# Performance work log

Measured on AMD Instinct MI355X. Metric: run time of the kernel, lower is better.

## Reference

```python
import jax, jax.numpy as jnp
import numpy as np

N_HEAD = 12
HEAD_DIM = 64
ROPE_THETA = 10000.0


def _rope_tables(t):
    half = HEAD_DIM // 2
    inv_freq = 1.0 / (ROPE_THETA ** (jnp.arange(0, HEAD_DIM, 2, dtype=jnp.float32) / HEAD_DIM))
    freqs = jnp.arange(t, dtype=jnp.float32)[:, None] * inv_freq[None, :]  # [t, half]
    return jnp.cos(freqs), jnp.sin(freqs)


def _apply_rope(q, k, cos, sin):
    # q,k: [b,h,t,d]; cos,sin: [t,d/2]
    half = HEAD_DIM // 2
    c = cos[None, None]
    s = sin[None, None]
    q1, q2 = q[..., :half], q[..., half:]
    k1, k2 = k[..., :half], k[..., half:]
    q = jnp.concatenate([q1 * c - q2 * s, q2 * c + q1 * s], axis=-1)
    k = jnp.concatenate([k1 * c - k2 * s, k2 * c + k1 * s], axis=-1)
    return q, k


def setup_inputs() -> dict:
    key = jax.random.key(0)
    ks = jax.random.split(key, 5)
    b, t, c = 1, 2048, 768
    return {
        "x": jax.random.normal(ks[0], (b, t, c), dtype=jnp.float32),
        "w_qkv": jax.random.normal(ks[1], (c, 3 * c), dtype=jnp.float32) * (1.0 / np.sqrt(c)),
        "b_qkv": jax.random.normal(ks[2], (3 * c,), dtype=jnp.float32) * 0.02,
        "w_proj": jax.random.normal(ks[3], (c, c), dtype=jnp.float32) * (1.0 / np.sqrt(c)),
        "b_proj": jax.random.normal(ks[4], (c,), dtype=jnp.float32) * 0.02,
    }


def reference(x, w_qkv, b_qkv, w_proj, b_proj):
    b, t, c = x.shape
    scale = 1.0 / np.sqrt(HEAD_DIM)
    qkv = jnp.einsum('btc,cd->btd', x, w_qkv) + b_qkv  # [b,t,3c]
    q, k, v = jnp.split(qkv, 3, axis=-1)
    # [b,t,c] -> [b,h,t,d]
    to_heads = lambda z: z.reshape(b, t, N_HEAD, HEAD_DIM).transpose(0, 2, 1, 3)
    q, k, v = to_heads(q), to_heads(k), to_heads(v)
    cos, sin = _rope_tables(t)
    q, k = _apply_rope(q, k, cos, sin)
    att = jnp.einsum('bhqd,bhkd->bhqk', q, k) * scale
    causal = jnp.tril(jnp.ones((t, t), dtype=bool))
    att = jnp.where(causal[None, None], att, -jnp.inf)
    att = jax.nn.softmax(att, axis=-1)
    y = jnp.einsum('bhqk,bhkd->bhqd', att, v)
    y = y.transpose(0, 2, 1, 3).reshape(b, t, c)
    return jnp.einsum('btc,cd->btd', y, w_proj) + b_proj
```

## Files before the change

### kernel.cpp

```cpp
#include <hip/hip_runtime.h>
#include <hip/hip_bf16.h>
#include <math.h>

#define T_SEQ 2048
#define C_DIM 768
#define NH    12
#define HD    64
#define QKV_N 2304
#define CH    4
#define NJOBS 1728

typedef __attribute__((ext_vector_type(8))) short short8;
typedef __attribute__((ext_vector_type(4))) short short4_t;
typedef __attribute__((ext_vector_type(4))) float f32x4;
typedef __hip_bfloat16 bf16;

static __device__ __forceinline__ unsigned int f2bf(float x) {
    bf16 b = __float2bfloat16(x);
    return (unsigned int)*reinterpret_cast<unsigned short*>(&b);
}
static __device__ __forceinline__ float bf2f(short u) {
    unsigned int v = ((unsigned int)(unsigned short)u) << 16;
    return *reinterpret_cast<float*>(&v);
}

static __device__ __forceinline__ void gload_lds16(const void* g, void* l) {
    __builtin_amdgcn_global_load_lds(
        (const __attribute__((address_space(1))) void*)g,
        (__attribute__((address_space(3))) void*)l, 16, 0, 0);
}

static __device__ __forceinline__ void transpose_tile(
    const float* __restrict__ W, short* __restrict__ Wt, int K, int N,
    int bx, int by, float* tile ) {
    int k0 = by * 64, n0 = bx * 64;
    int tid = threadIdx.x;
    #pragma unroll
    for (int e = 0; e < 16; ++e) {
        int idx = e * 256 + tid;
        int r = idx >> 6, c = idx & 63;
        tile[r * 65 + c] = W[(size_t)(k0 + r) * N + n0 + c];
    }
    __syncthreads();
    #pragma unroll
    for (int e = 0; e < 16; ++e) {
        int idx = e * 256 + tid;
        int n = idx >> 6, k = idx & 63;
        Wt[(size_t)(n0 + n) * K + k0 + k] = (short)f2bf(tile[k * 65 + n]);
    }
}

__global__ __launch_bounds__(256) void prep_kernel(
    const float* __restrict__ x, const float* __restrict__ w_qkv,
    const float* __restrict__ w_proj, short* __restrict__ xb,
    short* __restrict__ wqkvT, short* __restrict__ wprojT,
    float* __restrict__ ctab, float* __restrict__ stab) {
    __shared__ float tile[64 * 65];
    int b = blockIdx.x;
    int tid = threadIdx.x;
    if (b < 1536) {
        int idx = (b * 256 + tid) * 4;
        float4 v = *(const float4*)(x + idx);
        short4_t o;
        o[0] = (short)f2bf(v.x); o[1] = (short)f2bf(v.y);
        o[2] = (short)f2bf(v.z); o[3] = (short)f2bf(v.w);
        *(short4_t*)(xb + idx) = o;
    } else if (b < 1968) {
        int i = b - 1536;
        transpose_tile(w_qkv, wqkvT, C_DIM, QKV_N, i % 36, i / 36, tile);
    } else if (b < 2112) {
        int i = b - 1968;
        transpose_tile(w_proj, wprojT, C_DIM, C_DIM, i % 12, i / 12, tile);
    } else {
        int idx = (b - 2112) * 256 + tid;
        int p = idx >> 5;
        int i = idx & 31;
        float invf = exp2f(-(float)i * (0.03125f * 13.287712379549449f));
        float f = (float)p * invf;
        ctab[idx] = cosf(f);
        stab[idx] = sinf(f);
    }
}

__global__ __launch_bounds__(256) void gemm_qkv_rope_kernel(
    const short* __restrict__ A, const short* __restrict__ Bt,
    const float* __restrict__ bias, const float* __restrict__ ctab,
    const float* __restrict__ stab, short* __restrict__ Qout,
    short* __restrict__ Kout, short* __restrict__ Vtout) {
    __shared__ __align__(16) short smem[2 * 8 * 130 * 8];
    short* As = smem;
    short* Bs = smem + 8 * 130 * 8;
    int tid = threadIdx.x;
    int w = tid >> 6, l = tid & 63;
    int lr = l & 15, lg = l >> 4;
    int wm = w >> 1, wn = w & 1;
    int m0 = blockIdx.y * 128, n0 = blockIdx.x * 128;
    const int K = C_DIM;

    f32x4 acc[4][4] = {};

    for (int k0 = 0; k0 < K; k0 += 64) {
        __syncthreads();
        #pragma unroll
        for (int e = 0; e < 4; ++e) {
            int u = w * 4 + e;
            int kc = u >> 1, r0 = (u & 1) * 64;
            const short* srcA = A  + (size_t)(m0 + r0 + l) * K + k0 + kc * 8;
            const short* srcB = Bt + (size_t)(n0 + r0 + l) * K + k0 + kc * 8;
            gload_lds16(srcA, &As[(kc * 130 + r0) * 8]);
            gload_lds16(srcB, &Bs[(kc * 130 + r0) * 8]);
        }
        __syncthreads();
        #pragma unroll
        for (int ks = 0; ks < 2; ++ks) {
            short8 af[4], bf[4];
            #pragma unroll
            for (int mt = 0; mt < 4; ++mt)
                af[mt] = *(const short8*)&As[((ks * 4 + lg) * 130 + wm * 64 + mt * 16 + lr) * 8];
            #pragma unroll
            for (int nt = 0; nt < 4; ++nt)
                bf[nt] = *(const short8*)&Bs[((ks * 4 + lg) * 130 + wn * 64 + nt * 16 + lr) * 8];
            #pragma unroll
            for (int mt = 0; mt < 4; ++mt)
                #pragma unroll
                for (int nt = 0; nt < 4; ++nt)
                    acc[mt][nt] = __builtin_amdgcn_mfma_f32_16x16x32_bf16(
                        af[mt], bf[nt], acc[mt][nt], 0, 0, 0);
        }
    }

    __syncthreads();

    int nc0 = n0 + wn * 64;
    int tensor = nc0 / 768;
    int h = (nc0 - tensor * 768) >> 6;
    int t0g = m0 + wm * 64;

    float bv[4];
    #pragma unroll
    for (int nt = 0; nt < 4; ++nt) bv[nt] = bias[nc0 + nt * 16 + lr];

    if (tensor < 2) {
        short* dst = (tensor == 0 ? Qout : Kout) + (size_t)h * T_SEQ * HD;
        float qs = (tensor == 0) ? 0.125f : 1.0f;
        #pragma unroll
        for (int mt = 0; mt < 4; ++mt)
            #pragma unroll
            for (int r = 0; r < 4; ++r) {
                int t = t0g + mt * 16 + lg * 4 + r;
                #pragma unroll
                for (int nt = 0; nt < 2; ++nt) {
                    int i = nt * 16 + lr;
                    float c = ctab[t * 32 + i];
                    float s = stab[t * 32 + i];
                    float lo = acc[mt][nt][r]     + bv[nt];
                    float hi = acc[mt][nt + 2][r] + bv[nt + 2];
                    dst[(size_t)t * HD + i]      = (short)f2bf((lo * c - hi * s) * qs);
                    dst[(size_t)t * HD + i + 32] = (short)f2bf((hi * c + lo * s) * qs);
                }
            }
    } else {
        short* S = smem + w * 4096;
        #pragma unroll
        for (int mt = 0; mt < 4; ++mt)
            #pragma unroll
            for (int nt = 0; nt < 4; ++nt) {
                int d = nt * 16 + lr;
                #pragma unroll
                for (int r = 0; r < 4; ++r) {
                    int tl = mt * 16 + lg * 4 + r;
                    float v = acc[mt][nt][r] + bv[nt];
                    S[d * 64 + ((tl & 7) | (((tl >> 3) ^ (d & 7)) << 3))] =
                        (short)f2bf(v);
                }
            }
        asm volatile("s_waitcnt lgkmcnt(0)" ::: "memory");
        int cc = l & 7, db = l >> 3;
        #pragma unroll
        for (int i = 0; i < 8; ++i) {
            int d = db + i * 8;
            short8 v = *(const short8*)&S[d * 64 + ((cc ^ (d & 7)) << 3)];
            *(short8*)(Vtout + ((size_t)h * HD + d) * T_SEQ + t0g + cc * 8) = v;
        }
    }
}

__global__ __launch_bounds__(256) void gemm_proj_kernel(
    const short* __restrict__ A, const short* __restrict__ Bt,
    const float* __restrict__ bias, float* __restrict__ C) {
    const int K = C_DIM, N = C_DIM;
    __shared__ __align__(16) short As[8 * 66 * 8];
    __shared__ __align__(16) short Bs[8 * 66 * 8];
    int tid = threadIdx.x;
    int w = tid >> 6, l = tid & 63;
    int lr = l & 15, lg = l >> 4;
    int wm = w >> 1, wn = w & 1;
    int m0 = blockIdx.y * 64, n0 = blockIdx.x * 64;

    f32x4 acc[2][2] = {};

    for (int k0 = 0; k0 < K; k0 += 64) {
        __syncthreads();
        #pragma unroll
        for (int e = 0; e < 2; ++e) {
            int kc = w * 2 + e;
            gload_lds16(A  + (size_t)(m0 + l) * K + k0 + kc * 8, &As[kc * 66 * 8]);
            gload_lds16(Bt + (size_t)(n0 + l) * K + k0 + kc * 8, &Bs[kc * 66 * 8]);
        }
        __syncthreads();
        #pragma unroll
        for (int ks = 0; ks < 2; ++ks) {
            short8 af[2], bf[2];
            #pragma unroll
            for (int mt = 0; mt < 2; ++mt)
                af[mt] = *(const short8*)&As[((ks * 4 + lg) * 66 + wm * 32 + mt * 16 + lr) * 8];
            #pragma unroll
            for (int nt = 0; nt < 2; ++nt)
                bf[nt] = *(const short8*)&Bs[((ks * 4 + lg) * 66 + wn * 32 + nt * 16 + lr) * 8];
            #pragma unroll
            for (int mt = 0; mt < 2; ++mt)
                #pragma unroll
                for (int nt = 0; nt < 2; ++nt)
                    acc[mt][nt] = __builtin_amdgcn_mfma_f32_16x16x32_bf16(
                        af[mt], bf[nt], acc[mt][nt], 0, 0, 0);
        }
    }

    #pragma unroll
    for (int mt = 0; mt < 2; ++mt)
        #pragma unroll
        for (int r = 0; r < 4; ++r) {
            int row = m0 + wm * 32 + mt * 16 + lg * 4 + r;
            #pragma unroll
            for (int nt = 0; nt < 2; ++nt) {
                int col = n0 + wn * 32 + nt * 16 + lr;
                C[(size_t)row * N + col] = acc[mt][nt][r] + bias[col];
            }
        }
}

__global__ __launch_bounds__(256) void attn_mfma_kernel(
    const bf16* __restrict__ Qp, const bf16* __restrict__ Kp,
    const bf16* __restrict__ Vtp, short* __restrict__ Yb,
    short* __restrict__ Opart, float* __restrict__ ml) {
    __shared__ __align__(16) short KsB[2][64 * 64];
    __shared__ __align__(16) short VtB[2][64 * 64];
    __shared__ __align__(16) short Pl[4][16 * 64];

    int tid = threadIdx.x;
    int w  = tid >> 6;
    int l  = tid & 63;
    int lr = l & 15;
    int lg = l >> 4;

    int job = (NJOBS - 1) - blockIdx.x;
    int h = job % NH;
    int u = job / NH;
    int g = 0;
    while (u >= 2 * (g + 1) * (g + 2)) ++g;
    int v  = u - 2 * g * (g + 1);
    int jq = v / (g + 1);
    int qi = 4 * g + jq;
    int c0 = v - jq * (g + 1);
    int nch = g + 1;
    int kt0 = c0 * CH;
    int kt1 = kt0 + CH; if (kt1 > qi + 1) kt1 = qi + 1;
    int qt0 = qi * 64;

    const short* Qg  = (const short*)(Qp + (size_t)h * T_SEQ * HD);
    const short* Kg  = (const short*)(Kp + (size_t)h * T_SEQ * HD);
    const short* Vtg = (const short*)(Vtp + (size_t)h * HD * T_SEQ);

    int qrow = qt0 + w * 16 + lr;
    short8 qf0 = *(const short8*)(Qg + (size_t)qrow * HD + lg * 8);
    short8 qf1 = *(const short8*)(Qg + (size_t)qrow * HD + 32 + lg * 8);

    int srow = l >> 3;
    int cx   = (l & 7) ^ srow;

    auto stage = [&](int buf, int kt) {
        int k0 = kt * 64;
        #pragma unroll
        for (int e = 0; e < 2; ++e) {
            int r = e * 32 + w * 8 + srow;
            gload_lds16(Kg + (size_t)(k0 + r) * HD + cx * 8,
                        &KsB[buf][(e * 256 + w * 64) * 8]);
            gload_lds16(Vtg + (size_t)r * T_SEQ + k0 + cx * 8,
                        &VtB[buf][(e * 256 + w * 64) * 8]);
        }
    };

    f32x4 o[4] = {};
    float m = -INFINITY, lsum = 0.f;

    stage(0, kt0);

    for (int kt = kt0; kt < kt1; ++kt) {
        int cur = (kt - kt0) & 1;
        if (kt + 1 < kt1) {
            stage(1 - cur, kt + 1);
            asm volatile("s_waitcnt vmcnt(4)" ::: "memory");
        } else {
            asm volatile("s_waitcnt vmcnt(0)" ::: "memory");
        }
        __builtin_amdgcn_s_barrier();

        const short* Ks = KsB[cur];
        const short* Vt = VtB[cur];

        f32x4 c[4];
        #pragma unroll
        for (int mt = 0; mt < 4; ++mt) {
            c[mt] = (f32x4){0.f, 0.f, 0.f, 0.f};
            int row = mt * 16 + lr;
            #pragma unroll
            for (int ks = 0; ks < 2; ++ks) {
                short8 af = *(const short8*)(&Ks[row * 64 + (((ks * 4 + lg) ^ (row & 7)) << 3)]);
                c[mt] = __builtin_amdgcn_mfma_f32_16x16x32_bf16(af, ks ? qf1 : qf0, c[mt], 0, 0, 0);
            }
        }

        float p[16];
        float smax = -INFINITY;
        if (kt == qi) {
            int qg = qt0 + w * 16 + lr;
            int k0 = kt * 64;
            #pragma unroll
            for (int mt = 0; mt < 4; ++mt)
                #pragma unroll
                for (int r = 0; r < 4; ++r) {
                    float s = c[mt][r];
                    if (k0 + mt * 16 + lg * 4 + r > qg) s = -INFINITY;
                    p[mt * 4 + r] = s;
                    smax = fmaxf(smax, s);
                }
        } else {
            #pragma unroll
            for (int mt = 0; mt < 4; ++mt)
                #pragma unroll
                for (int r = 0; r < 4; ++r) {
                    float s = c[mt][r];
                    p[mt * 4 + r] = s;
                    smax = fmaxf(smax, s);
                }
        }
        smax = fmaxf(smax, __shfl_xor(smax, 16));
        smax = fmaxf(smax, __shfl_xor(smax, 32));
        float mnew = fmaxf(m, smax);
        float alpha = __expf(m - mnew);
        float ps = 0.f;
        #pragma unroll
        for (int i = 0; i < 16; ++i) { p[i] = __expf(p[i] - mnew); ps += p[i]; }
        ps += __shfl_xor(ps, 16);
        ps += __shfl_xor(ps, 32);
        lsum = lsum * alpha + ps;
        m = mnew;

        #pragma unroll
        for (int r = 0; r < 4; ++r) {
            float ar = __shfl(alpha, lg * 4 + r);
            #pragma unroll
            for (int nt = 0; nt < 4; ++nt) o[nt][r] *= ar;
        }

        short* Pw = &Pl[w][0];
        #pragma unroll
        for (int mt = 0; mt < 4; ++mt)
            #pragma unroll
            for (int rh = 0; rh < 2; ++rh) {
                unsigned int uu = f2bf(p[mt * 4 + 2 * rh]) | (f2bf(p[mt * 4 + 2 * rh + 1]) << 16);
                int chunk = 2 * mt + (lg >> 1);
                *(unsigned int*)(&Pw[lr * 64 + ((chunk ^ (lr & 7)) << 3)
                                     + 4 * (lg & 1) + 2 * rh]) = uu;
            }
        asm volatile("" ::: "memory");

        #pragma unroll
        for (int ks = 0; ks < 2; ++ks) {
            short8 pf = *(const short8*)(&Pw[lr * 64 + (((ks * 4 + lg) ^ (lr & 7)) << 3)]);
            #pragma unroll
            for (int nt = 0; nt < 4; ++nt) {
                int vrow = nt * 16 + lr;
                short8 vf = *(const short8*)(&Vt[vrow * 64 + (((ks * 4 + lg) ^ (vrow & 7)) << 3)]);
                o[nt] = __builtin_amdgcn_mfma_f32_16x16x32_bf16(pf, vf, o[nt], 0, 0, 0);
            }
        }
        __builtin_amdgcn_s_barrier();
    }

    if (nch == 1) {
        float invl = 1.f / lsum;
        #pragma unroll
        for (int r = 0; r < 4; ++r) {
            float ir = __shfl(invl, lg * 4 + r);
            int row = qt0 + w * 16 + lg * 4 + r;
            #pragma unroll
            for (int nt = 0; nt < 4; ++nt)
                Yb[(size_t)row * C_DIM + h * HD + nt * 16 + lr] =
                    (short)f2bf(o[nt][r] * ir);
        }
    } else {
        if (lg == 0) {
            ml[(size_t)job * 128 + w * 16 + lr] = m;
            ml[(size_t)job * 128 + 64 + w * 16 + lr] = lsum;
        }
        #pragma unroll
        for (int r = 0; r < 4; ++r) {
            int row = w * 16 + lg * 4 + r;
            #pragma unroll
            for (int nt = 0; nt < 4; ++nt)
                Opart[(size_t)job * 4096 + row * 64 + nt * 16 + lr] =
                    (short)f2bf(o[nt][r]);
        }
    }
}

__global__ __launch_bounds__(256) void combine_kernel(
    const short* __restrict__ Opart, const float* __restrict__ ml,
    short* __restrict__ Yb) {
    int job = blockIdx.x;
    int h  = job % NH;
    int qi = 4 + job / NH;
    int g  = qi >> 2;
    int nch = g + 1;
    int u0 = (g + 1) * (qi - 2 * g);

    int tid = threadIdx.x;
    int row = tid >> 2;
    int qp  = tid & 3;

    float mm[8], ll[8];
    float M = -INFINITY;
    #pragma unroll
    for (int c = 0; c < 8; ++c) {
        mm[c] = -INFINITY; ll[c] = 0.f;
        if (c < nch) {
            size_t pidx = (size_t)(u0 + c) * NH + h;
            mm[c] = ml[pidx * 128 + row];
            ll[c] = ml[pidx * 128 + 64 + row];
            M = fmaxf(M, mm[c]);
        }
    }
    float acc[16] = {};
    float L = 0.f;
    #pragma unroll
    for (int c = 0; c < 8; ++c) {
        if (c < nch) {
            float wgt = __expf(mm[c] - M);
            L += ll[c] * wgt;
            const short* op = Opart + ((size_t)(u0 + c) * NH + h) * 4096
                            + row * 64 + qp * 16;
            short8 a = *(const short8*)op;
            short8 b = *(const short8*)(op + 8);
            #pragma unroll
            for (int j = 0; j < 8; ++j) {
                acc[j]     += wgt * bf2f(a[j]);
                acc[8 + j] += wgt * bf2f(b[j]);
            }
        }
    }
    float invL = 1.f / L;
    short8 oa, ob;
    #pragma unroll
    for (int j = 0; j < 8; ++j) {
        oa[j] = (short)f2bf(acc[j] * invL);
        ob[j] = (short)f2bf(acc[8 + j] * invL);
    }
    short* dst = Yb + (size_t)(qi * 64 + row) * C_DIM + h * HD + qp * 16;
    *(short8*)dst = oa;
    *(short8*)(dst + 8) = ob;
}

extern "C" void kernel_launch(void* const* d_in, const int* in_sizes, int n_in,
                              void* d_out, int out_size, void* d_ws, size_t ws_size,
                              hipStream_t stream) {
    const float* x      = (const float*)d_in[0];
    const float* w_qkv  = (const float*)d_in[1];
    const float* b_qkv  = (const float*)d_in[2];
    const float* w_proj = (const float*)d_in[3];
    const float* b_proj = (const float*)d_in[4];
    float* out = (float*)d_out;

    float* ws = (float*)d_ws;
    short* yb     = (short*)ws;
    short* wprojT = (short*)(ws + 786432);
    short* Opart  = (short*)(ws + 1081344);
    float* mlbuf  = ws + 4620288;
    short* Qh     = (short*)(ws + 4841472);
    short* Kh     = (short*)(ws + 5627904);
    short* Vt     = (short*)(ws + 6414336);
    float* ctab   = ws + 7200768;
    float* stab   = ws + 7266304;
    short* xb     = (short*)(ws + 7331840);
    short* wqkvT  = (short*)(ws + 8118272);

    prep_kernel<<<2368, 256, 0, stream>>>(x, w_qkv, w_proj, xb, wqkvT, wprojT,
                                          ctab, stab);

    dim3 g1(QKV_N / 128, T_SEQ / 128);
    gemm_qkv_rope_kernel<<<g1, 256, 0, stream>>>(xb, wqkvT, b_qkv, ctab, stab,
                                                 Qh, Kh, Vt);

    attn_mfma_kernel<<<NJOBS, 256, 0, stream>>>((const bf16*)Qh, (const bf16*)Kh,
                                                (const bf16*)Vt, yb, Opart, mlbuf);

    combine_kernel<<<NH * 28, 256, 0, stream>>>(Opart, mlbuf, yb);

    dim3 g4(C_DIM / 64, T_SEQ / 64);
    gemm_proj_kernel<<<g4, 256, 0, stream>>>(yb, wprojT, b_proj, out);
}
```

Baseline: 83.25 us.

## Double-buffer LDS tiles in QKV and projection GEMMs with async prefetch

Both the QKV+RoPE GEMM and the output projection GEMM now keep two LDS buffers and issue the global-to-LDS loads for the next K-step before computing on the current one. Explicit vmcnt waits and raw s_barrier calls replace the per-step __syncthreads pairs. The goal is to hide global load latency behind MFMA work. In exchange the LDS footprint doubles, which may lower occupancy, and correctness depends on the hand-tuned vmcnt counts matching the number of outstanding loads.

```diff
diff --git a/kernel.cpp b/kernel.cpp
--- a/kernel.cpp
+++ b/kernel.cpp
@@ -82,14 +82,13 @@
     }
 }
 
+#define QSTRIDE 8320
 __global__ __launch_bounds__(256) void gemm_qkv_rope_kernel(
     const short* __restrict__ A, const short* __restrict__ Bt,
     const float* __restrict__ bias, const float* __restrict__ ctab,
     const float* __restrict__ stab, short* __restrict__ Qout,
     short* __restrict__ Kout, short* __restrict__ Vtout) {
-    __shared__ __align__(16) short smem[2 * 8 * 130 * 8];
-    short* As = smem;
-    short* Bs = smem + 8 * 130 * 8;
+    __shared__ __align__(16) short smem[4 * QSTRIDE];
     int tid = threadIdx.x;
     int w = tid >> 6, l = tid & 63;
     int lr = l & 15, lg = l >> 4;
@@ -99,18 +98,35 @@
 
     f32x4 acc[4][4] = {};
 
-    for (int k0 = 0; k0 < K; k0 += 64) {
-        __syncthreads();
+    auto stage = [&](int buf, int k0) {
+        short* dstA = smem + buf * 2 * QSTRIDE;
+        short* dstB = dstA + QSTRIDE;
         #pragma unroll
         for (int e = 0; e < 4; ++e) {
             int u = w * 4 + e;
             int kc = u >> 1, r0 = (u & 1) * 64;
-            const short* srcA = A  + (size_t)(m0 + r0 + l) * K + k0 + kc * 8;
-            const short* srcB = Bt + (size_t)(n0 + r0 + l) * K + k0 + kc * 8;
-            gload_lds16(srcA, &As[(kc * 130 + r0) * 8]);
-            gload_lds16(srcB, &Bs[(kc * 130 + r0) * 8]);
-        }
-        __syncthreads();
+            gload_lds16(A  + (size_t)(m0 + r0 + l) * K + k0 + kc * 8,
+                        &dstA[(kc * 130 + r0) * 8]);
+            gload_lds16(Bt + (size_t)(n0 + r0 + l) * K + k0 + kc * 8,
+                        &dstB[(kc * 130 + r0) * 8]);
+        }
+    };
+
+    stage(0, 0);
+
+    for (int step = 0; step < K / 64; ++step) {
+        int cur = step & 1;
+        int k0n = (step + 1) * 64;
+        if (k0n < K) {
+            stage(1 - cur, k0n);
+            asm volatile("s_waitcnt vmcnt(8)" ::: "memory");
+        } else {
+            asm volatile("s_waitcnt vmcnt(0)" ::: "memory");
+        }
+        __builtin_amdgcn_s_barrier();
+
+        const short* As = smem + cur * 2 * QSTRIDE;
+        const short* Bs = As + QSTRIDE;
         #pragma unroll
         for (int ks = 0; ks < 2; ++ks) {
             short8 af[4], bf[4];
@@ -127,9 +143,8 @@
                     acc[mt][nt] = __builtin_amdgcn_mfma_f32_16x16x32_bf16(
                         af[mt], bf[nt], acc[mt][nt], 0, 0, 0);
         }
-    }
-
-    __syncthreads();
+        __builtin_amdgcn_s_barrier();
+    }
 
     int nc0 = n0 + wn * 64;
     int tensor = nc0 / 768;
@@ -185,12 +200,12 @@
     }
 }
 
+#define PSTRIDE 4224
 __global__ __launch_bounds__(256) void gemm_proj_kernel(
     const short* __restrict__ A, const short* __restrict__ Bt,
     const float* __restrict__ bias, float* __restrict__ C) {
     const int K = C_DIM, N = C_DIM;
-    __shared__ __align__(16) short As[8 * 66 * 8];
-    __shared__ __align__(16) short Bs[8 * 66 * 8];
+    __shared__ __align__(16) short smem[4 * PSTRIDE];
     int tid = threadIdx.x;
     int w = tid >> 6, l = tid & 63;
     int lr = l & 15, lg = l >> 4;
@@ -199,15 +214,32 @@
 
     f32x4 acc[2][2] = {};
 
-    for (int k0 = 0; k0 < K; k0 += 64) {
-        __syncthreads();
+    auto stage = [&](int buf, int k0) {
+        short* dstA = smem + buf * 2 * PSTRIDE;
+        short* dstB = dstA + PSTRIDE;
         #pragma unroll
         for (int e = 0; e < 2; ++e) {
             int kc = w * 2 + e;
-            gload_lds16(A  + (size_t)(m0 + l) * K + k0 + kc * 8, &As[kc * 66 * 8]);
-            gload_lds16(Bt + (size_t)(n0 + l) * K + k0 + kc * 8, &Bs[kc * 66 * 8]);
-        }
-        __syncthreads();
+            gload_lds16(A  + (size_t)(m0 + l) * K + k0 + kc * 8, &dstA[kc * 66 * 8]);
+            gload_lds16(Bt + (size_t)(n0 + l) * K + k0 + kc * 8, &dstB[kc * 66 * 8]);
+        }
+    };
+
+    stage(0, 0);
+
+    for (int step = 0; step < K / 64; ++step) {
+        int cur = step & 1;
+        int k0n = (step + 1) * 64;
+        if (k0n < K) {
+            stage(1 - cur, k0n);
+            asm volatile("s_waitcnt vmcnt(4)" ::: "memory");
+        } else {
+            asm volatile("s_waitcnt vmcnt(0)" ::: "memory");
+        }
+        __builtin_amdgcn_s_barrier();
+
+        const short* As = smem + cur * 2 * PSTRIDE;
+        const short* Bs = As + PSTRIDE;
         #pragma unroll
         for (int ks = 0; ks < 2; ++ks) {
             short8 af[2], bf[2];
@@ -224,6 +256,7 @@
                     acc[mt][nt] = __builtin_amdgcn_mfma_f32_16x16x32_bf16(
                         af[mt], bf[nt], acc[mt][nt], 0, 0, 0);
         }
+        __builtin_amdgcn_s_barrier();
     }
 
     #pragma unroll
```

Result: slower. 86.33 us (+3.7%).

## Enlarge attention query tile to 128 rows per block, halving job count

Applied to the files above, without the earlier changes.

Each attention block now processes 128 query rows (two 16-row sub-tiles per wave) instead of 64, so every staged K/V tile in LDS is reused by twice as many MFMAs. The job decomposition, split-KV chunk indexing, partial output layout and combine kernel are rewritten for the new tile size. This halves the K/V global traffic per query row, at the cost of more registers per wave, fewer blocks (864 instead of 1728) for load balance, and masking work on diagonal tiles now spread across two key tiles.

```diff
diff --git a/kernel.cpp b/kernel.cpp
--- a/kernel.cpp
+++ b/kernel.cpp
@@ -8,7 +8,7 @@
 #define HD    64
 #define QKV_N 2304
 #define CH    4
-#define NJOBS 1728
+#define NJOBS 864
 
 typedef __attribute__((ext_vector_type(8))) short short8;
 typedef __attribute__((ext_vector_type(4))) short short4_t;
@@ -245,7 +245,7 @@
     short* __restrict__ Opart, float* __restrict__ ml) {
     __shared__ __align__(16) short KsB[2][64 * 64];
     __shared__ __align__(16) short VtB[2][64 * 64];
-    __shared__ __align__(16) short Pl[4][16 * 64];
+    __shared__ __align__(16) short Pl[4][2][16 * 64];
 
     int tid = threadIdx.x;
     int w  = tid >> 6;
@@ -256,24 +256,27 @@
     int job = (NJOBS - 1) - blockIdx.x;
     int h = job % NH;
     int u = job / NH;
-    int g = 0;
-    while (u >= 2 * (g + 1) * (g + 2)) ++g;
-    int v  = u - 2 * g * (g + 1);
-    int jq = v / (g + 1);
-    int qi = 4 * g + jq;
-    int c0 = v - jq * (g + 1);
-    int nch = g + 1;
+    int a = 0;
+    while (u >= (a + 1) * (a + 2)) ++a;
+    int rem = u - a * (a + 1);
+    int qi2, c0;
+    if (rem < a + 1) { qi2 = 2 * a;     c0 = rem; }
+    else             { qi2 = 2 * a + 1; c0 = rem - (a + 1); }
+    int nch = a + 1;
+    int ntile = 2 * qi2 + 2;
     int kt0 = c0 * CH;
-    int kt1 = kt0 + CH; if (kt1 > qi + 1) kt1 = qi + 1;
-    int qt0 = qi * 64;
+    int kt1 = kt0 + CH; if (kt1 > ntile) kt1 = ntile;
+    int qt0 = qi2 * 128;
 
     const short* Qg  = (const short*)(Qp + (size_t)h * T_SEQ * HD);
     const short* Kg  = (const short*)(Kp + (size_t)h * T_SEQ * HD);
     const short* Vtg = (const short*)(Vtp + (size_t)h * HD * T_SEQ);
 
-    int qrow = qt0 + w * 16 + lr;
-    short8 qf0 = *(const short8*)(Qg + (size_t)qrow * HD + lg * 8);
-    short8 qf1 = *(const short8*)(Qg + (size_t)qrow * HD + 32 + lg * 8);
+    int q0 = qt0 + w * 32 + lr;
+    short8 qA0 = *(const short8*)(Qg + (size_t)q0 * HD + lg * 8);
+    short8 qA1 = *(const short8*)(Qg + (size_t)q0 * HD + 32 + lg * 8);
+    short8 qB0 = *(const short8*)(Qg + (size_t)(q0 + 16) * HD + lg * 8);
+    short8 qB1 = *(const short8*)(Qg + (size_t)(q0 + 16) * HD + 32 + lg * 8);
 
     int srow = l >> 3;
     int cx   = (l & 7) ^ srow;
@@ -290,8 +293,8 @@
         }
     };
 
-    f32x4 o[4] = {};
-    float m = -INFINITY, lsum = 0.f;
+    f32x4 oA[4] = {}, oB[4] = {};
+    float mA = -INFINITY, lA = 0.f, mB = -INFINITY, lB = 0.f;
 
     stage(0, kt0);
 
@@ -307,110 +310,119 @@
 
         const short* Ks = KsB[cur];
         const short* Vt = VtB[cur];
-
-        f32x4 c[4];
+        int k0 = kt * 64;
+
+        f32x4 cA[4], cB[4];
         #pragma unroll
         for (int mt = 0; mt < 4; ++mt) {
-            c[mt] = (f32x4){0.f, 0.f, 0.f, 0.f};
+            cA[mt] = (f32x4){0.f, 0.f, 0.f, 0.f};
+            cB[mt] = (f32x4){0.f, 0.f, 0.f, 0.f};
             int row = mt * 16 + lr;
             #pragma unroll
             for (int ks = 0; ks < 2; ++ks) {
                 short8 af = *(const short8*)(&Ks[row * 64 + (((ks * 4 + lg) ^ (row & 7)) << 3)]);
-                c[mt] = __builtin_amdgcn_mfma_f32_16x16x32_bf16(af, ks ? qf1 : qf0, c[mt], 0, 0, 0);
-            }
-        }
-
-        float p[16];
-        float smax = -INFINITY;
-        if (kt == qi) {
-            int qg = qt0 + w * 16 + lr;
-            int k0 = kt * 64;
+                cA[mt] = __builtin_amdgcn_mfma_f32_16x16x32_bf16(af, ks ? qA1 : qA0, cA[mt], 0, 0, 0);
+                cB[mt] = __builtin_amdgcn_mfma_f32_16x16x32_bf16(af, ks ? qB1 : qB0, cB[mt], 0, 0, 0);
+            }
+        }
+
+        auto sm = [&](f32x4* c, int base, float& m, float& lsum, f32x4* o,
+                      short* Pw) {
+            int qg = base + lr;
+            bool domask = (k0 + 63) > base;
+            float p[16];
+            float smax = -INFINITY;
             #pragma unroll
             for (int mt = 0; mt < 4; ++mt)
                 #pragma unroll
                 for (int r = 0; r < 4; ++r) {
                     float s = c[mt][r];
-                    if (k0 + mt * 16 + lg * 4 + r > qg) s = -INFINITY;
+                    if (domask && (k0 + mt * 16 + lg * 4 + r > qg)) s = -INFINITY;
                     p[mt * 4 + r] = s;
                     smax = fmaxf(smax, s);
                 }
-        } else {
+            smax = fmaxf(smax, __shfl_xor(smax, 16));
+            smax = fmaxf(smax, __shfl_xor(smax, 32));
+            float mnew = fmaxf(m, smax);
+            float alpha = __expf(m - mnew);
+            float ps = 0.f;
+            #pragma unroll
+            for (int i = 0; i < 16; ++i) { p[i] = __expf(p[i] - mnew); ps += p[i]; }
+            ps += __shfl_xor(ps, 16);
+            ps += __shfl_xor(ps, 32);
+            lsum = lsum * alpha + ps;
+            m = mnew;
+            #pragma unroll
+            for (int r = 0; r < 4; ++r) {
+                float ar = __shfl(alpha, lg * 4 + r);
+                #pragma unroll
+                for (int nt = 0; nt < 4; ++nt) o[nt][r] *= ar;
+            }
             #pragma unroll
             for (int mt = 0; mt < 4; ++mt)
                 #pragma unroll
-                for (int r = 0; r < 4; ++r) {
-                    float s = c[mt][r];
-                    p[mt * 4 + r] = s;
-                    smax = fmaxf(smax, s);
+                for (int rh = 0; rh < 2; ++rh) {
+                    unsigned int uu = f2bf(p[mt * 4 + 2 * rh])
+                                    | (f2bf(p[mt * 4 + 2 * rh + 1]) << 16);
+                    int chunk = 2 * mt + (lg >> 1);
+                    *(unsigned int*)(&Pw[lr * 64 + ((chunk ^ (lr & 7)) << 3)
+                                         + 4 * (lg & 1) + 2 * rh]) = uu;
                 }
-        }
-        smax = fmaxf(smax, __shfl_xor(smax, 16));
-        smax = fmaxf(smax, __shfl_xor(smax, 32));
-        float mnew = fmaxf(m, smax);
-        float alpha = __expf(m - mnew);
-        float ps = 0.f;
-        #pragma unroll
-        for (int i = 0; i < 16; ++i) { p[i] = __expf(p[i] - mnew); ps += p[i]; }
-        ps += __shfl_xor(ps, 16);
-        ps += __shfl_xor(ps, 32);
-        lsum = lsum * alpha + ps;
-        m = mnew;
-
-        #pragma unroll
-        for (int r = 0; r < 4; ++r) {
-            float ar = __shfl(alpha, lg * 4 + r);
-            #pragma unroll
-            for (int nt = 0; nt < 4; ++nt) o[nt][r] *= ar;
-        }
-
-        short* Pw = &Pl[w][0];
-        #pragma unroll
-        for (int mt = 0; mt < 4; ++mt)
-            #pragma unroll
-            for (int rh = 0; rh < 2; ++rh) {
-                unsigned int uu = f2bf(p[mt * 4 + 2 * rh]) | (f2bf(p[mt * 4 + 2 * rh + 1]) << 16);
-                int chunk = 2 * mt + (lg >> 1);
-                *(unsigned int*)(&Pw[lr * 64 + ((chunk ^ (lr & 7)) << 3)
-                                     + 4 * (lg & 1) + 2 * rh]) = uu;
-            }
+        };
+        sm(cA, qt0 + w * 32,      mA, lA, oA, &Pl[w][0][0]);
+        sm(cB, qt0 + w * 32 + 16, mB, lB, oB, &Pl[w][1][0]);
         asm volatile("" ::: "memory");
 
         #pragma unroll
         for (int ks = 0; ks < 2; ++ks) {
-            short8 pf = *(const short8*)(&Pw[lr * 64 + (((ks * 4 + lg) ^ (lr & 7)) << 3)]);
+            int po = (((ks * 4 + lg) ^ (lr & 7)) << 3);
+            short8 pfA = *(const short8*)(&Pl[w][0][lr * 64 + po]);
+            short8 pfB = *(const short8*)(&Pl[w][1][lr * 64 + po]);
             #pragma unroll
             for (int nt = 0; nt < 4; ++nt) {
                 int vrow = nt * 16 + lr;
                 short8 vf = *(const short8*)(&Vt[vrow * 64 + (((ks * 4 + lg) ^ (vrow & 7)) << 3)]);
-                o[nt] = __builtin_amdgcn_mfma_f32_16x16x32_bf16(pf, vf, o[nt], 0, 0, 0);
+                oA[nt] = __builtin_amdgcn_mfma_f32_16x16x32_bf16(pfA, vf, oA[nt], 0, 0, 0);
+                oB[nt] = __builtin_amdgcn_mfma_f32_16x16x32_bf16(pfB, vf, oB[nt], 0, 0, 0);
             }
         }
         __builtin_amdgcn_s_barrier();
     }
 
     if (nch == 1) {
-        float invl = 1.f / lsum;
+        float invA = 1.f / lA, invB = 1.f / lB;
         #pragma unroll
         for (int r = 0; r < 4; ++r) {
-            float ir = __shfl(invl, lg * 4 + r);
-            int row = qt0 + w * 16 + lg * 4 + r;
-            #pragma unroll
-            for (int nt = 0; nt < 4; ++nt)
-                Yb[(size_t)row * C_DIM + h * HD + nt * 16 + lr] =
-                    (short)f2bf(o[nt][r] * ir);
+            float irA = __shfl(invA, lg * 4 + r);
+            float irB = __shfl(invB, lg * 4 + r);
+            int rowA = qt0 + w * 32 + lg * 4 + r;
+            #pragma unroll
+            for (int nt = 0; nt < 4; ++nt) {
+                Yb[(size_t)rowA * C_DIM + h * HD + nt * 16 + lr] =
+                    (short)f2bf(oA[nt][r] * irA);
+                Yb[(size_t)(rowA + 16) * C_DIM + h * HD + nt * 16 + lr] =
+                    (short)f2bf(oB[nt][r] * irB);
+            }
         }
     } else {
         if (lg == 0) {
-            ml[(size_t)job * 128 + w * 16 + lr] = m;
-            ml[(size_t)job * 128 + 64 + w * 16 + lr] = lsum;
+            int rA = w * 32 + lr;
+            ml[(size_t)job * 256 + (rA >> 6) * 128 + (rA & 63)] = mA;
+            ml[(size_t)job * 256 + (rA >> 6) * 128 + 64 + (rA & 63)] = lA;
+            int rB = rA + 16;
+            ml[(size_t)job * 256 + (rB >> 6) * 128 + (rB & 63)] = mB;
+            ml[(size_t)job * 256 + (rB >> 6) * 128 + 64 + (rB & 63)] = lB;
         }
         #pragma unroll
         for (int r = 0; r < 4; ++r) {
-            int row = w * 16 + lg * 4 + r;
-            #pragma unroll
-            for (int nt = 0; nt < 4; ++nt)
-                Opart[(size_t)job * 4096 + row * 64 + nt * 16 + lr] =
-                    (short)f2bf(o[nt][r]);
+            int rowA = w * 32 + lg * 4 + r;
+            #pragma unroll
+            for (int nt = 0; nt < 4; ++nt) {
+                Opart[(size_t)job * 8192 + rowA * 64 + nt * 16 + lr] =
+                    (short)f2bf(oA[nt][r]);
+                Opart[(size_t)job * 8192 + (rowA + 16) * 64 + nt * 16 + lr] =
+                    (short)f2bf(oB[nt][r]);
+            }
         }
     }
 }
@@ -419,11 +431,13 @@
     const short* __restrict__ Opart, const float* __restrict__ ml,
     short* __restrict__ Yb) {
     int job = blockIdx.x;
-    int h  = job % NH;
-    int qi = 4 + job / NH;
-    int g  = qi >> 2;
-    int nch = g + 1;
-    int u0 = (g + 1) * (qi - 2 * g);
+    int h    = job % NH;
+    int qi64 = 4 + job / NH;
+    int qi2  = qi64 >> 1;
+    int rh   = qi64 & 1;
+    int a    = qi2 >> 1;
+    int nch  = a + 1;
+    int u0   = a * (a + 1) + (qi2 & 1) * (a + 1);
 
     int tid = threadIdx.x;
     int row = tid >> 2;
@@ -435,9 +449,9 @@
     for (int c = 0; c < 8; ++c) {
         mm[c] = -INFINITY; ll[c] = 0.f;
         if (c < nch) {
-            size_t pidx = (size_t)(u0 + c) * NH + h;
-            mm[c] = ml[pidx * 128 + row];
-            ll[c] = ml[pidx * 128 + 64 + row];
+            size_t pj = (size_t)(u0 + c) * NH + h;
+            mm[c] = ml[pj * 256 + rh * 128 + row];
+            ll[c] = ml[pj * 256 + rh * 128 + 64 + row];
             M = fmaxf(M, mm[c]);
         }
     }
@@ -448,14 +462,14 @@
         if (c < nch) {
             float wgt = __expf(mm[c] - M);
             L += ll[c] * wgt;
-            const short* op = Opart + ((size_t)(u0 + c) * NH + h) * 4096
-                            + row * 64 + qp * 16;
-            short8 a = *(const short8*)op;
-            short8 b = *(const short8*)(op + 8);
+            const short* op = Opart + ((size_t)(u0 + c) * NH + h) * 8192
+                            + (rh * 64 + row) * 64 + qp * 16;
+            short8 va = *(const short8*)op;
+            short8 vb = *(const short8*)(op + 8);
             #pragma unroll
             for (int j = 0; j < 8; ++j) {
-                acc[j]     += wgt * bf2f(a[j]);
-                acc[8 + j] += wgt * bf2f(b[j]);
+                acc[j]     += wgt * bf2f(va[j]);
+                acc[8 + j] += wgt * bf2f(vb[j]);
             }
         }
     }
@@ -466,7 +480,7 @@
         oa[j] = (short)f2bf(acc[j] * invL);
         ob[j] = (short)f2bf(acc[8 + j] * invL);
     }
-    short* dst = Yb + (size_t)(qi * 64 + row) * C_DIM + h * HD + qp * 16;
+    short* dst = Yb + (size_t)(qi64 * 64 + row) * C_DIM + h * HD + qp * 16;
     *(short8*)dst = oa;
     *(short8*)(dst + 8) = ob;
 }
```

Measured after the change: 88.19 us. 1.06x slower.
